# Optimization experiments

Hardware: AMD Instinct MI355X
Metric: run time of the kernel (lower is better)

The kernel has to match this reference:

```python
import jax, jax.numpy as jnp
import numpy as np

N = 500000   # total nodes
C = 128      # input_features
R = 4        # reduction
B = 32       # batch_num (graphs)


def setup_inputs() -> dict:
    key = jax.random.key(0)
    k0, k1, k2, k3, k4, k5 = jax.random.split(key, 6)
    x_input = jax.random.normal(k0, (N, C), dtype=jnp.float32)
    batch = jnp.sort(jax.random.randint(k1, (N,), 0, B)).astype(jnp.int64)
    # SE gate MLP params: Linear(C, C//R) -> ReLU -> Linear(C//R, C)
    W1 = jax.random.normal(k2, (C, C // R), dtype=jnp.float32) * (1.0 / np.sqrt(C))
    b1 = jax.random.normal(k3, (C // R,), dtype=jnp.float32) * 0.01
    W2 = jax.random.normal(k4, (C // R, C), dtype=jnp.float32) * (1.0 / np.sqrt(C // R))
    b2 = jax.random.normal(k5, (C,), dtype=jnp.float32) * 0.01
    return {"x_input": x_input, "batch": batch, "batch_num": B,
            "W1": W1, "b1": b1, "W2": W2, "b2": b2}


def reference(x_input, batch, batch_num, W1, b1, W2, b2):
    # segment mean pool over graphs (global_mean_pool)
    sums = jax.ops.segment_sum(x_input, batch, num_segments=batch_num)          # [B, C]
    counts = jax.ops.segment_sum(jnp.ones((x_input.shape[0],), x_input.dtype),
                                 batch, num_segments=batch_num)                  # [B]
    avg = sums / jnp.maximum(counts, 1.0)[:, None]
    # 2-layer MLP gate + sigmoid
    h = jax.nn.relu(avg @ W1 + b1)
    attn = jax.nn.sigmoid(h @ W2 + b2)                                           # [B, C]
    # per-node broadcast multiply (gather attn by graph id)
    return x_input * attn[batch]
```

## Files before the change

### kernel.cpp

```cpp
#include <hip/hip_runtime.h>
#include <hip/hip_bf16.h>

#define C 128
#define CR 32
#define B 32
#define RPB 256

typedef float f32x4 __attribute__((ext_vector_type(4)));

__device__ inline int lower_bound_i(const int* __restrict__ a, int n, int key) {
    int lo = 0, hi = n;
    while (lo < hi) {
        int mid = (lo + hi) >> 1;
        if (a[mid] < key) lo = mid + 1; else hi = mid;
    }
    return lo;
}

__global__ __launch_bounds__(256) void seg_partial_kernel(
    const f32x4* __restrict__ x4, const int* __restrict__ batch,
    f32x4* __restrict__ partial4, int N)
{
    const int t  = threadIdx.x;
    const int c4 = t & 31;
    const int rl = t >> 5;
    const long base = (long)blockIdx.x * RPB;
    long rend = base + RPB;
    if (rend > N) rend = N;

    if (batch[base] != batch[rend - 1]) return;

    const f32x4* p = x4 + (base + rl) * 32 + c4;
    long r = base + rl;
    f32x4 acc0 = (f32x4)(0.f), acc1 = (f32x4)(0.f);
    f32x4 acc2 = (f32x4)(0.f), acc3 = (f32x4)(0.f);
    while (r + 56 < rend) {
        f32x4 v0 = p[0 * 256];
        f32x4 v1 = p[1 * 256];
        f32x4 v2 = p[2 * 256];
        f32x4 v3 = p[3 * 256];
        f32x4 v4 = p[4 * 256];
        f32x4 v5 = p[5 * 256];
        f32x4 v6 = p[6 * 256];
        f32x4 v7 = p[7 * 256];
        acc0 += v0; acc1 += v1; acc2 += v2; acc3 += v3;
        acc0 += v4; acc1 += v5; acc2 += v6; acc3 += v7;
        r += 64; p += 8 * 256;
    }
    while (r < rend) { acc0 += p[0]; r += 8; p += 256; }
    f32x4 acc = (acc0 + acc1) + (acc2 + acc3);

    __shared__ f32x4 s_red[8][32];
    s_red[rl][c4] = acc;
    __syncthreads();
    if (t < 32) {
        f32x4 s = s_red[0][t];
        #pragma unroll
        for (int i = 1; i < 8; ++i) s += s_red[i][t];
        partial4[(long)blockIdx.x * 32 + t] = s;
    }
}

__global__ __launch_bounds__(1024) void reduce_mlp_kernel(
    const f32x4* __restrict__ x4, const int* __restrict__ batch,
    const f32x4* __restrict__ partial4,
    const float* __restrict__ W1, const float* __restrict__ b1,
    const float* __restrict__ W2, const float* __restrict__ b2,
    float* __restrict__ attn, int N)
{
    const int seg = blockIdx.x;
    const int t   = threadIdx.x;
    const int c4  = t & 31;
    const int rl  = t >> 5;

    const int lo = lower_bound_i(batch, N, seg);
    const int hi = lower_bound_i(batch, N, seg + 1);

    f32x4 acc = (f32x4)(0.f);
    const int fb0 = (lo + RPB - 1) / RPB;
    const int fb1 = hi / RPB;
    if (fb0 < fb1) {
        for (int blk = fb0 + rl; blk < fb1; blk += 32)
            acc += partial4[(long)blk * 32 + c4];
        #pragma unroll 4
        for (long r = lo + rl; r < (long)fb0 * RPB; r += 32)
            acc += x4[r * 32 + c4];
        #pragma unroll 4
        for (long r = (long)fb1 * RPB + rl; r < hi; r += 32)
            acc += x4[r * 32 + c4];
    } else {
        #pragma unroll 4
        for (long r = lo + rl; r < hi; r += 32)
            acc += x4[r * 32 + c4];
    }

    __shared__ f32x4 s_red[32][32];
    __shared__ float s_avg[C];
    __shared__ float s_h[CR];
    s_red[rl][c4] = acc;
    __syncthreads();
    if (t < 32) {
        f32x4 s = s_red[0][t];
        #pragma unroll
        for (int i = 1; i < 32; ++i) s += s_red[i][t];
        float inv = 1.0f / fmaxf((float)(hi - lo), 1.0f);
        s_avg[4 * t + 0] = s.x * inv;
        s_avg[4 * t + 1] = s.y * inv;
        s_avg[4 * t + 2] = s.z * inv;
        s_avg[4 * t + 3] = s.w * inv;
    }
    __syncthreads();
    if (t < CR) {
        float d = b1[t];
        #pragma unroll 8
        for (int c = 0; c < C; ++c)
            d += s_avg[c] * W1[c * CR + t];
        s_h[t] = fmaxf(d, 0.f);
    }
    __syncthreads();
    if (t < C) {
        float d = b2[t];
        #pragma unroll
        for (int j = 0; j < CR; ++j)
            d += s_h[j] * W2[j * C + t];
        attn[seg * C + t] = 1.0f / (1.0f + expf(-d));
    }
}

__global__ __launch_bounds__(256) void scale_kernel(
    const f32x4* __restrict__ x4, const int* __restrict__ batch,
    const f32x4* __restrict__ attn4, f32x4* __restrict__ out4,
    long total4)
{
    long idx    = (long)blockIdx.x * blockDim.x + threadIdx.x;
    long stride = (long)gridDim.x * blockDim.x;
    for (; idx < total4; idx += stride) {
        long row = idx >> 5;
        int  c4  = (int)(idx & 31);
        int  b   = batch[row];
        f32x4 xv = x4[idx];
        f32x4 av = attn4[b * 32 + c4];
        f32x4 o  = xv * av;
        __builtin_nontemporal_store(o, &out4[idx]);
    }
}

extern "C" void kernel_launch(void* const* d_in, const int* in_sizes, int n_in,
                              void* d_out, int out_size, void* d_ws, size_t ws_size,
                              hipStream_t stream) {
    const float* x     = (const float*)d_in[0];
    const int*   batch = (const int*)d_in[1];
    const float* W1 = (const float*)d_in[3];
    const float* b1 = (const float*)d_in[4];
    const float* W2 = (const float*)d_in[5];
    const float* b2 = (const float*)d_in[6];
    float* out = (float*)d_out;

    const int N = in_sizes[0] / C;
    const int nblocks = (N + RPB - 1) / RPB;

    float* attn    = (float*)d_ws;
    float* partial = attn + B * C;

    seg_partial_kernel<<<nblocks, 256, 0, stream>>>((const f32x4*)x, batch,
                                                    (f32x4*)partial, N);

    reduce_mlp_kernel<<<B, 1024, 0, stream>>>((const f32x4*)x, batch,
                                              (const f32x4*)partial,
                                              W1, b1, W2, b2, attn, N);

    const long total4 = (long)N * (C / 4);
    scale_kernel<<<2048, 256, 0, stream>>>((const f32x4*)x, batch,
                                           (const f32x4*)attn, (f32x4*)out, total4);
}
```

Measured before the change: 134.2 us.

## Fuse segment reduction, MLP gate and scaling into one cooperative kernel

```diff
diff --git a/kernel.cpp b/kernel.cpp
--- a/kernel.cpp
+++ b/kernel.cpp
@@ -1,12 +1,14 @@
 #include <hip/hip_runtime.h>
-#include <hip/hip_bf16.h>
+#include <hip/hip_cooperative_groups.h>
 
 #define C 128
 #define CR 32
 #define B 32
 #define RPB 256
+#define NTHR 256
 
 typedef float f32x4 __attribute__((ext_vector_type(4)));
+namespace cg = cooperative_groups;
 
 __device__ inline int lower_bound_i(const int* __restrict__ a, int n, int key) {
     int lo = 0, hi = n;
@@ -15,6 +17,145 @@
         if (a[mid] < key) lo = mid + 1; else hi = mid;
     }
     return lo;
+}
+
+__global__ __launch_bounds__(NTHR, 2) void fused_se_kernel(
+    const f32x4* __restrict__ x4, const int* __restrict__ batch,
+    const float* __restrict__ W1, const float* __restrict__ b1,
+    const float* __restrict__ W2, const float* __restrict__ b2,
+    f32x4* __restrict__ partial4, float* __restrict__ attn,
+    f32x4* __restrict__ out4, int N)
+{
+    cg::grid_group grid = cg::this_grid();
+    const int t  = threadIdx.x;
+    const int c4 = t & 31;
+    const int rl = t >> 5;
+    const int ntiles = (N + RPB - 1) / RPB;
+
+    __shared__ f32x4 s_redA[8][32];
+    __shared__ f32x4 s_redB[8][32];
+
+    for (int tile = blockIdx.x; tile < ntiles; tile += gridDim.x) {
+        const long base = (long)tile * RPB;
+        long rend = base + RPB;
+        if (rend > N) rend = N;
+        const int segA = batch[base];
+        const int segB = batch[rend - 1];
+
+        if (segA == segB) {
+            const f32x4* p = x4 + (base + rl) * 32 + c4;
+            long r = base + rl;
+            f32x4 a0 = (f32x4)(0.f), a1 = (f32x4)(0.f);
+            f32x4 a2 = (f32x4)(0.f), a3 = (f32x4)(0.f);
+            while (r + 56 < rend) {
+                f32x4 v0 = p[0 * 256];
+                f32x4 v1 = p[1 * 256];
+                f32x4 v2 = p[2 * 256];
+                f32x4 v3 = p[3 * 256];
+                f32x4 v4 = p[4 * 256];
+                f32x4 v5 = p[5 * 256];
+                f32x4 v6 = p[6 * 256];
+                f32x4 v7 = p[7 * 256];
+                a0 += v0; a1 += v1; a2 += v2; a3 += v3;
+                a0 += v4; a1 += v5; a2 += v6; a3 += v7;
+                r += 64; p += 8 * 256;
+            }
+            while (r < rend) { a0 += p[0]; r += 8; p += 256; }
+            f32x4 acc = (a0 + a1) + (a2 + a3);
+
+            s_redA[rl][c4] = acc;
+            __syncthreads();
+            if (t < 32) {
+                f32x4 s = s_redA[0][t];
+                #pragma unroll
+                for (int i = 1; i < 8; ++i) s += s_redA[i][t];
+                partial4[(long)tile * 64 + t] = s;
+            }
+            __syncthreads();
+        } else {
+            f32x4 accA = (f32x4)(0.f), accB = (f32x4)(0.f);
+            for (long r = base + rl; r < rend; r += 8) {
+                int b = batch[r];
+                f32x4 v = x4[r * 32 + c4];
+                if (b == segA) accA += v; else accB += v;
+            }
+            s_redA[rl][c4] = accA;
+            s_redB[rl][c4] = accB;
+            __syncthreads();
+            if (t < 32) {
+                f32x4 sA = s_redA[0][t], sB = s_redB[0][t];
+                #pragma unroll
+                for (int i = 1; i < 8; ++i) { sA += s_redA[i][t]; sB += s_redB[i][t]; }
+                partial4[(long)tile * 64 + t]      = sA;
+                partial4[(long)tile * 64 + 32 + t] = sB;
+            }
+            __syncthreads();
+        }
+    }
+
+    grid.sync();
+
+    if (blockIdx.x < B) {
+        const int seg = blockIdx.x;
+        const int lo = lower_bound_i(batch, N, seg);
+        const int hi = lower_bound_i(batch, N, seg + 1);
+
+        f32x4 acc = (f32x4)(0.f);
+        if (lo < hi) {
+            const int t0 = lo / RPB;
+            const int t1 = (hi - 1) / RPB;
+            const bool headoff = (lo & (RPB - 1)) != 0;
+            for (int tt = t0 + rl; tt <= t1; tt += 8) {
+                int slot = (tt == t0 && headoff) ? 1 : 0;
+                acc += partial4[(long)tt * 64 + slot * 32 + c4];
+            }
+        }
+        s_redA[rl][c4] = acc;
+        __syncthreads();
+
+        __shared__ float s_avg[C];
+        __shared__ float s_h[CR];
+        if (t < 32) {
+            f32x4 s = s_redA[0][t];
+            #pragma unroll
+            for (int i = 1; i < 8; ++i) s += s_redA[i][t];
+            float inv = 1.0f / fmaxf((float)(hi - lo), 1.0f);
+            s_avg[4 * t + 0] = s.x * inv;
+            s_avg[4 * t + 1] = s.y * inv;
+            s_avg[4 * t + 2] = s.z * inv;
+            s_avg[4 * t + 3] = s.w * inv;
+        }
+        __syncthreads();
+        if (t < CR) {
+            float d = b1[t];
+            #pragma unroll 8
+            for (int c = 0; c < C; ++c)
+                d += s_avg[c] * W1[c * CR + t];
+            s_h[t] = fmaxf(d, 0.f);
+        }
+        __syncthreads();
+        if (t < C) {
+            float d = b2[t];
+            #pragma unroll
+            for (int j = 0; j < CR; ++j)
+                d += s_h[j] * W2[j * C + t];
+            attn[seg * C + t] = 1.0f / (1.0f + expf(-d));
+        }
+    }
+
+    grid.sync();
+
+    const f32x4* __restrict__ attn4 = (const f32x4*)attn;
+    const long total4 = (long)N * 32;
+    long idx = (long)blockIdx.x * NTHR + t;
+    const long stride = (long)gridDim.x * NTHR;
+    for (; idx < total4; idx += stride) {
+        long row = idx >> 5;
+        int  cc  = (int)(idx & 31);
+        int  b   = batch[row];
+        f32x4 o = x4[idx] * attn4[b * 32 + cc];
+        __builtin_nontemporal_store(o, &out4[idx]);
+    }
 }
 
 __global__ __launch_bounds__(256) void seg_partial_kernel(
@@ -32,8 +173,8 @@
 
     const f32x4* p = x4 + (base + rl) * 32 + c4;
     long r = base + rl;
-    f32x4 acc0 = (f32x4)(0.f), acc1 = (f32x4)(0.f);
-    f32x4 acc2 = (f32x4)(0.f), acc3 = (f32x4)(0.f);
+    f32x4 a0 = (f32x4)(0.f), a1 = (f32x4)(0.f);
+    f32x4 a2 = (f32x4)(0.f), a3 = (f32x4)(0.f);
     while (r + 56 < rend) {
         f32x4 v0 = p[0 * 256];
         f32x4 v1 = p[1 * 256];
@@ -43,12 +184,12 @@
         f32x4 v5 = p[5 * 256];
         f32x4 v6 = p[6 * 256];
         f32x4 v7 = p[7 * 256];
-        acc0 += v0; acc1 += v1; acc2 += v2; acc3 += v3;
-        acc0 += v4; acc1 += v5; acc2 += v6; acc3 += v7;
+        a0 += v0; a1 += v1; a2 += v2; a3 += v3;
+        a0 += v4; a1 += v5; a2 += v6; a3 += v7;
         r += 64; p += 8 * 256;
     }
-    while (r < rend) { acc0 += p[0]; r += 8; p += 256; }
-    f32x4 acc = (acc0 + acc1) + (acc2 + acc3);
+    while (r < rend) { a0 += p[0]; r += 8; p += 256; }
+    f32x4 acc = (a0 + a1) + (a2 + a3);
 
     __shared__ f32x4 s_red[8][32];
     s_red[rl][c4] = acc;
@@ -138,9 +279,7 @@
         long row = idx >> 5;
         int  c4  = (int)(idx & 31);
         int  b   = batch[row];
-        f32x4 xv = x4[idx];
-        f32x4 av = attn4[b * 32 + c4];
-        f32x4 o  = xv * av;
+        f32x4 o = x4[idx] * attn4[b * 32 + c4];
         __builtin_nontemporal_store(o, &out4[idx]);
     }
 }
@@ -157,19 +296,43 @@
     float* out = (float*)d_out;
 
     const int N = in_sizes[0] / C;
-    const int nblocks = (N + RPB - 1) / RPB;
+    const int ntiles = (N + RPB - 1) / RPB;
 
     float* attn    = (float*)d_ws;
     float* partial = attn + B * C;
-
-    seg_partial_kernel<<<nblocks, 256, 0, stream>>>((const f32x4*)x, batch,
-                                                    (f32x4*)partial, N);
-
-    reduce_mlp_kernel<<<B, 1024, 0, stream>>>((const f32x4*)x, batch,
-                                              (const f32x4*)partial,
-                                              W1, b1, W2, b2, attn, N);
-
-    const long total4 = (long)N * (C / 4);
-    scale_kernel<<<2048, 256, 0, stream>>>((const f32x4*)x, batch,
-                                           (const f32x4*)attn, (f32x4*)out, total4);
-}
+    const size_t ws_needed = ((size_t)B * C + (size_t)ntiles * 2 * C) * sizeof(float);
+
+    bool coop_ok = false;
+    if (ws_size >= ws_needed) {
+        int maxBlocksPerCU = 0;
+        hipError_t oe = hipOccupancyMaxActiveBlocksPerMultiprocessor(
+            &maxBlocksPerCU, (const void*)fused_se_kernel, NTHR, 0);
+        if (oe == hipSuccess && maxBlocksPerCU > 0) {
+            int nblk = maxBlocksPerCU * 256;
+            if (nblk > 1024) nblk = 1024;
+            if (nblk >= B) {
+                void* args[] = {
+                    (void*)&x, (void*)&batch,
+                    (void*)&W1, (void*)&b1, (void*)&W2, (void*)&b2,
+                    (void*)&partial, (void*)&attn, (void*)&out, (void*)&N
+                };
+                hipError_t le = hipLaunchCooperativeKernel(
+                    (const void*)fused_se_kernel, dim3(nblk), dim3(NTHR),
+                    args, 0, stream);
+                coop_ok = (le == hipSuccess);
+            }
+        }
+    }
+
+    if (!coop_ok) {
+        seg_partial_kernel<<<ntiles, 256, 0, stream>>>((const f32x4*)x, batch,
+                                                       (f32x4*)partial, N);
+        reduce_mlp_kernel<<<B, 1024, 0, stream>>>((const f32x4*)x, batch,
+                                                  (const f32x4*)partial,
+                                                  W1, b1, W2, b2, attn, N);
+        const long total4 = (long)N * 32;
+        scale_kernel<<<2048, 256, 0, stream>>>((const f32x4*)x, batch,
+                                               (const f32x4*)attn, (f32x4*)out,
+                                               total4);
+    }
+}
```

Measured after the change: 329.4 us. 2.45x slower.
